# Kernel tuning notes

Hardware: AMD Instinct MI355X
Metric: run time of the kernel (lower is better)

Reference implementation:

```python
import jax, jax.numpy as jnp
import numpy as np

N_NODES = 100000
N_EDGES = 3200000
IN_CH = 64
HID = [64, 32, 16]


def setup_inputs() -> dict:
    key = jax.random.key(0)
    ks = jax.random.split(key, 12)
    x = jax.random.normal(ks[0], (N_NODES, IN_CH), dtype=jnp.float32)
    edge_index = jax.random.randint(ks[1], (2, N_EDGES), 0, N_NODES, dtype=jnp.int32)
    dims = [IN_CH] + HID
    params = {}
    i = 2
    for l in range(3):
        din, dout = dims[l], dims[l + 1]
        sc = 1.0 / np.sqrt(din)
        params[f"Wl{l}"] = jax.random.uniform(ks[i], (din, dout), jnp.float32, -sc, sc); i += 1
        params[f"Wr{l}"] = jax.random.uniform(ks[i], (din, dout), jnp.float32, -sc, sc); i += 1
        params[f"b{l}"] = jnp.zeros((dout,), jnp.float32)
    sc = 1.0 / np.sqrt(HID[-1])
    params["Wc"] = jax.random.uniform(ks[i], (HID[-1], 1), jnp.float32, -sc, sc)
    params["bc"] = jnp.zeros((1,), jnp.float32)
    return dict(x=x, edge_index=edge_index, **params)


def _sage_conv(x, src, dst, Wl, Wr, b):
    # message = x[src]; mean-aggregate at dst; out = agg @ Wl + x @ Wr + b
    msg = x[src]  # [E, din]
    s = jax.ops.segment_sum(msg, dst, num_segments=N_NODES)
    cnt = jax.ops.segment_sum(jnp.ones((dst.shape[0],), x.dtype), dst, num_segments=N_NODES)
    agg = s / jnp.maximum(cnt, 1.0)[:, None]
    return agg @ Wl + x @ Wr + b


def reference(x, edge_index, Wl0, Wr0, b0, Wl1, Wr1, b1, Wl2, Wr2, b2, Wc, bc):
    src, dst = edge_index[0], edge_index[1]
    h = jax.nn.relu(_sage_conv(x, src, dst, Wl0, Wr0, b0))
    h = jax.nn.relu(_sage_conv(h, src, dst, Wl1, Wr1, b1))
    h = jax.nn.relu(_sage_conv(h, src, dst, Wl2, Wr2, b2))
    return h @ Wc + bc  # [N_NODES, 1]
```

## Files before the change

### kernel.cpp

```cpp
#include <hip/hip_runtime.h>


#define NN 100000
#define BSH 8
#define NBK ((NN + 255) >> 8)
#define HB 256
#define SRCMASK 0x1FFFF
#define DLSH 17
#define SPCAP 12500
#define LADJ_CAP 10240

__device__ __forceinline__ unsigned f2bf(float f) {
    unsigned u = __float_as_uint(f);
    u += 0x7fffu + ((u >> 16) & 1u);
    return u >> 16;
}
__device__ __forceinline__ float bflo(unsigned u) { return __uint_as_float(u << 16); }
__device__ __forceinline__ float bfhi(unsigned u) { return __uint_as_float(u & 0xffff0000u); }

__global__ void part1_k(const int* __restrict__ src, const int* __restrict__ dst,
                        int E, int* __restrict__ gcnt, int* __restrict__ goff,
                        unsigned* __restrict__ pair) {
    __shared__ unsigned spair[SPCAP];
    __shared__ int lh[NBK];
    __shared__ int part[512];
    int c = blockIdx.x, tid = threadIdx.x;
    int chunk = (E + HB - 1) / HB;
    int b0 = c * chunk, e0 = min(b0 + chunk, E);
    int n = e0 - b0;
    if (tid < NBK) lh[tid] = 0;
    __syncthreads();
    for (int e = b0 + tid; e < e0; e += 512) atomicAdd(&lh[dst[e] >> BSH], 1);
    __syncthreads();
    int cnt = (tid < NBK) ? lh[tid] : 0;
    part[tid] = cnt;
    __syncthreads();
    for (int d = 1; d < 512; d <<= 1) {
        int t = (tid >= d) ? part[tid - d] : 0;
        __syncthreads();
        part[tid] += t;
        __syncthreads();
    }
    int run = (tid == 0) ? 0 : part[tid - 1];
    if (tid < NBK) {
        gcnt[(size_t)c * NBK + tid] = cnt;
        goff[(size_t)c * NBK + tid] = run;
        lh[tid] = run;
    }
    __syncthreads();
    for (int e = b0 + tid; e < e0; e += 512) {
        int dv = dst[e], sv = src[e];
        int p = atomicAdd(&lh[dv >> BSH], 1);
        spair[p] = (unsigned)sv | ((unsigned)(dv & 255) << DLSH);
    }
    __syncthreads();
    for (int i = tid; i < n; i += 512) pair[b0 + i] = spair[i];
}

__global__ void bsum_k(const int* __restrict__ gcnt, int* __restrict__ bb, int E) {
    __shared__ int part[512];
    int tid = threadIdx.x;
    int s = 0;
    if (tid < NBK)
        for (int c = 0; c < HB; ++c) s += gcnt[(size_t)c * NBK + tid];
    part[tid] = s;
    __syncthreads();
    for (int d = 1; d < 512; d <<= 1) {
        int t = (tid >= d) ? part[tid - d] : 0;
        __syncthreads();
        part[tid] += t;
        __syncthreads();
    }
    if (tid < NBK) bb[tid] = part[tid] - s;
    if (tid == 0) bb[NBK] = E;
}

__global__ void sort2_k(const unsigned* __restrict__ pair, const int* __restrict__ goff,
                        const int* __restrict__ bb, int* __restrict__ adj,
                        int* __restrict__ off, float* __restrict__ inv, int N, int E) {
    __shared__ int ladj[LADJ_CAP];
    __shared__ int sls[HB], sle[HB];
    __shared__ int lcur[256];
    __shared__ int part[256];
    int b = blockIdx.x, tid = threadIdx.x;
    int chunk = (E + HB - 1) / HB;
    int b0c = tid * chunk, e0c = min(b0c + chunk, E);
    int ls = b0c + goff[(size_t)tid * NBK + b];
    int le = (b + 1 < NBK) ? (b0c + goff[(size_t)tid * NBK + b + 1]) : e0c;
    sls[tid] = ls; sle[tid] = le;
    lcur[tid] = 0;
    __syncthreads();
    for (int i = ls; i < le; ++i)
        atomicAdd(&lcur[pair[i] >> DLSH], 1);
    __syncthreads();
    int cn = lcur[tid];
    part[tid] = cn;
    __syncthreads();
    for (int d = 1; d < 256; d <<= 1) {
        int t = (tid >= d) ? part[tid - d] : 0;
        __syncthreads();
        part[tid] += t;
        __syncthreads();
    }
    int run = part[tid] - cn;
    int base = bb[b];
    int total = bb[b + 1] - base;
    int v = (b << BSH) + tid;
    if (v < N) { off[v] = base + run; inv[v] = 1.f / (float)max(cn, 1); }
    if (b == NBK - 1 && tid == 0) off[N] = E;
    lcur[tid] = run;
    __syncthreads();
    for (int i = sls[tid]; i < sle[tid]; ++i) {
        unsigned u = pair[i];
        int p = atomicAdd(&lcur[u >> DLSH], 1);
        int val = u & SRCMASK;
        if (p < LADJ_CAP) ladj[p] = val;
        else adj[base + p] = val;
    }
    __syncthreads();
    int lim = min(total, LADJ_CAP);
    for (int i = tid; i < lim; i += 256) adj[base + i] = ladj[i];
}

template <int DIN, int DOUT>
__global__ void transform2_k(const float* __restrict__ h,
                             const float* __restrict__ Wl, const float* __restrict__ Wr,
                             const float* __restrict__ bias,
                             unsigned* __restrict__ g, float2* __restrict__ r, int N) {
    constexpr int JP = DOUT / 2;
    __shared__ float2 sWl[DIN * JP];
    __shared__ float2 sWr[DIN * JP];
    __shared__ float2 sb[JP];
    const float2* Wl2 = (const float2*)Wl;
    const float2* Wr2 = (const float2*)Wr;
    for (int i = threadIdx.x; i < DIN * JP; i += blockDim.x) { sWl[i] = Wl2[i]; sWr[i] = Wr2[i]; }
    if (threadIdx.x < JP) sb[threadIdx.x] = ((const float2*)bias)[threadIdx.x];
    __syncthreads();
    int idx = blockIdx.x * blockDim.x + threadIdx.x;
    int NP = N / 2;
    if (idx >= NP * JP) return;
    int p = idx / JP, jp = idx % JP;
    int v0 = 2 * p, v1 = v0 + 1;
    const float* h0 = h + (size_t)v0 * DIN;
    const float* h1 = h + (size_t)v1 * DIN;
    float gl0x = 0, gl0y = 0, gl1x = 0, gl1y = 0;
    float gr0x = 0, gr0y = 0, gr1x = 0, gr1y = 0;
#pragma unroll
    for (int k = 0; k < DIN; ++k) {
        float2 wl = sWl[k * JP + jp];
        float2 wr = sWr[k * JP + jp];
        float a0 = h0[k], a1 = h1[k];
        gl0x = fmaf(a0, wl.x, gl0x); gl0y = fmaf(a0, wl.y, gl0y);
        gl1x = fmaf(a1, wl.x, gl1x); gl1y = fmaf(a1, wl.y, gl1y);
        gr0x = fmaf(a0, wr.x, gr0x); gr0y = fmaf(a0, wr.y, gr0y);
        gr1x = fmaf(a1, wr.x, gr1x); gr1y = fmaf(a1, wr.y, gr1y);
    }
    float2 bb = sb[jp];
    g[(size_t)v0 * JP + jp] = f2bf(gl0x) | (f2bf(gl0y) << 16);
    g[(size_t)v1 * JP + jp] = f2bf(gl1x) | (f2bf(gl1y) << 16);
    r[(size_t)v0 * JP + jp] = make_float2(gr0x + bb.x, gr0y + bb.y);
    r[(size_t)v1 * JP + jp] = make_float2(gr1x + bb.x, gr1y + bb.y);
}

template <int DOUT, int WAVES, int HEAD>
__global__ void agg_k(const unsigned* __restrict__ g, const int* __restrict__ off,
                      const int* __restrict__ adj, const float* __restrict__ invc,
                      const float* r, const float* __restrict__ Wc,
                      const float* __restrict__ bc, float* out, int N) {
    constexpr int Q8 = DOUT / 8;
    constexpr int EPT = 64 / Q8;
    __shared__ float sagg[WAVES][DOUT];
    int wid = threadIdx.x >> 6, lane = threadIdx.x & 63;
    int v = blockIdx.x * WAVES + wid;
    bool active = v < N;
    int q = lane & (Q8 - 1);
    int eg = lane / Q8;
    float acc[8] = {0, 0, 0, 0, 0, 0, 0, 0};
#define ACCU(U) do { \
        acc[0] += bflo(U.x); acc[1] += bfhi(U.x); \
        acc[2] += bflo(U.y); acc[3] += bfhi(U.y); \
        acc[4] += bflo(U.z); acc[5] += bfhi(U.z); \
        acc[6] += bflo(U.w); acc[7] += bfhi(U.w); } while (0)
    if (active) {
        int beg = off[v], end = off[v + 1];
        const uint4* g4 = (const uint4*)g;
        int i = beg + eg;
        for (; i + 3 * EPT < end; i += 4 * EPT) {
            int s0 = adj[i], s1 = adj[i + EPT], s2 = adj[i + 2 * EPT], s3 = adj[i + 3 * EPT];
            uint4 u0 = g4[(size_t)s0 * Q8 + q];
            uint4 u1 = g4[(size_t)s1 * Q8 + q];
            uint4 u2 = g4[(size_t)s2 * Q8 + q];
            uint4 u3 = g4[(size_t)s3 * Q8 + q];
            ACCU(u0); ACCU(u1); ACCU(u2); ACCU(u3);
        }
        for (; i < end; i += EPT) {
            int sv = adj[i];
            uint4 u = g4[(size_t)sv * Q8 + q];
            ACCU(u);
        }
#pragma unroll
        for (int d = Q8; d < 64; d <<= 1)
#pragma unroll
            for (int c = 0; c < 8; ++c) acc[c] += __shfl_xor(acc[c], d, 64);
        if (eg == 0) {
            float4* sp = (float4*)&sagg[wid][q * 8];
            sp[0] = make_float4(acc[0], acc[1], acc[2], acc[3]);
            sp[1] = make_float4(acc[4], acc[5], acc[6], acc[7]);
        }
    }
#undef ACCU
    __syncthreads();
    if (active && lane < DOUT) {
        float iv = invc[v];
        float val = fmaxf(fmaf(sagg[wid][lane], iv, r[(size_t)v * DOUT + lane]), 0.f);
        if (!HEAD) {
            out[(size_t)v * DOUT + lane] = val;
        } else {
            float pp = val * Wc[lane];
#pragma unroll
            for (int d = 1; d < 16; d <<= 1) pp += __shfl_xor(pp, d, 64);
            if (lane == 0) out[v] = pp + bc[0];
        }
    }
}

extern "C" void kernel_launch(void* const* d_in, const int* in_sizes, int n_in,
                              void* d_out, int out_size, void* d_ws, size_t ws_size,
                              hipStream_t stream) {
    const float* x   = (const float*)d_in[0];
    const int*   ei  = (const int*)d_in[1];
    const float* Wl0 = (const float*)d_in[2];
    const float* Wr0 = (const float*)d_in[3];
    const float* b0  = (const float*)d_in[4];
    const float* Wl1 = (const float*)d_in[5];
    const float* Wr1 = (const float*)d_in[6];
    const float* b1  = (const float*)d_in[7];
    const float* Wl2 = (const float*)d_in[8];
    const float* Wr2 = (const float*)d_in[9];
    const float* b2  = (const float*)d_in[10];
    const float* Wc  = (const float*)d_in[11];
    const float* bc  = (const float*)d_in[12];
    float* out = (float*)d_out;

    const int N = NN;
    const int E = in_sizes[1] / 2;
    const int* src = ei;
    const int* dst = ei + E;

    char* ws = (char*)d_ws;
    const size_t MB = 1 << 20;
    int*      gcnt = (int*)(ws + 0);
    int*      goff = (int*)(ws + 1 * MB);
    int*      bb   = (int*)(ws + 2 * MB);
    int*      off  = (int*)(ws + 3 * MB);
    float*    inv  = (float*)(ws + 3 * MB + 512 * 1024);
    unsigned* pair = (unsigned*)(ws + 4 * MB);
    int*      adj  = (int*)(ws + 17 * MB);
    unsigned* g0 = (unsigned*)(ws + 30 * MB);
    float*    r0 = (float*)(ws + 43 * MB);
    float*    h1 = r0;
    unsigned* g1 = (unsigned*)(ws + 4 * MB);
    float*    r1 = (float*)(ws + 30 * MB);
    float*    h2 = r1;
    unsigned* g2 = (unsigned*)(ws + 11 * MB);
    float*    r2 = (float*)(ws + 43 * MB);

    part1_k<<<HB, 512, 0, stream>>>(src, dst, E, gcnt, goff, pair);
    bsum_k<<<1, 512, 0, stream>>>(gcnt, bb, E);
    sort2_k<<<NBK, HB, 0, stream>>>(pair, goff, bb, adj, off, inv, N, E);

    transform2_k<64, 64><<<(N / 2 * 32 + 255) / 256, 256, 0, stream>>>(x, Wl0, Wr0, b0, g0, (float2*)r0, N);
    agg_k<64, 4, 0><<<(N + 3) / 4, 256, 0, stream>>>(g0, off, adj, inv, r0, nullptr, nullptr, h1, N);

    transform2_k<64, 32><<<(N / 2 * 16 + 255) / 256, 256, 0, stream>>>(h1, Wl1, Wr1, b1, g1, (float2*)r1, N);
    agg_k<32, 4, 0><<<(N + 3) / 4, 256, 0, stream>>>(g1, off, adj, inv, r1, nullptr, nullptr, h2, N);

    transform2_k<32, 16><<<(N / 2 * 8 + 255) / 256, 256, 0, stream>>>(h2, Wl2, Wr2, b2, g2, (float2*)r2, N);
    agg_k<16, 4, 1><<<(N + 3) / 4, 256, 0, stream>>>(g2, off, adj, inv, r2, Wc, bc, out, N);
}
```

Before: 405.4 us.

## Fuse next-layer transform into aggregation kernels and store residual in bf16

```diff
diff --git a/kernel.cpp b/kernel.cpp
--- a/kernel.cpp
+++ b/kernel.cpp
@@ -17,11 +17,13 @@
 }
 __device__ __forceinline__ float bflo(unsigned u) { return __uint_as_float(u << 16); }
 __device__ __forceinline__ float bfhi(unsigned u) { return __uint_as_float(u & 0xffff0000u); }
+__device__ __forceinline__ float bfs(unsigned short s) { return __uint_as_float((unsigned)s << 16); }
 
 __global__ void part1_k(const int* __restrict__ src, const int* __restrict__ dst,
                         int E, int* __restrict__ gcnt, int* __restrict__ goff,
                         unsigned* __restrict__ pair) {
     __shared__ unsigned spair[SPCAP];
+    __shared__ int sdst[SPCAP];
     __shared__ int lh[NBK];
     __shared__ int part[512];
     int c = blockIdx.x, tid = threadIdx.x;
@@ -30,7 +32,11 @@
     int n = e0 - b0;
     if (tid < NBK) lh[tid] = 0;
     __syncthreads();
-    for (int e = b0 + tid; e < e0; e += 512) atomicAdd(&lh[dst[e] >> BSH], 1);
+    for (int i = tid; i < n; i += 512) {
+        int dv = dst[b0 + i];
+        sdst[i] = dv;
+        atomicAdd(&lh[dv >> BSH], 1);
+    }
     __syncthreads();
     int cnt = (tid < NBK) ? lh[tid] : 0;
     part[tid] = cnt;
@@ -48,8 +54,9 @@
         lh[tid] = run;
     }
     __syncthreads();
-    for (int e = b0 + tid; e < e0; e += 512) {
-        int dv = dst[e], sv = src[e];
+    for (int i = tid; i < n; i += 512) {
+        int dv = sdst[i];
+        int sv = src[b0 + i];
         int p = atomicAdd(&lh[dv >> BSH], 1);
         spair[p] = (unsigned)sv | ((unsigned)(dv & 255) << DLSH);
     }
@@ -126,7 +133,7 @@
 __global__ void transform2_k(const float* __restrict__ h,
                              const float* __restrict__ Wl, const float* __restrict__ Wr,
                              const float* __restrict__ bias,
-                             unsigned* __restrict__ g, float2* __restrict__ r, int N) {
+                             unsigned* __restrict__ g, unsigned* __restrict__ r, int N) {
     constexpr int JP = DOUT / 2;
     __shared__ float2 sWl[DIN * JP];
     __shared__ float2 sWr[DIN * JP];
@@ -158,18 +165,27 @@
     float2 bb = sb[jp];
     g[(size_t)v0 * JP + jp] = f2bf(gl0x) | (f2bf(gl0y) << 16);
     g[(size_t)v1 * JP + jp] = f2bf(gl1x) | (f2bf(gl1y) << 16);
-    r[(size_t)v0 * JP + jp] = make_float2(gr0x + bb.x, gr0y + bb.y);
-    r[(size_t)v1 * JP + jp] = make_float2(gr1x + bb.x, gr1y + bb.y);
-}
-
-template <int DOUT, int WAVES, int HEAD>
-__global__ void agg_k(const unsigned* __restrict__ g, const int* __restrict__ off,
-                      const int* __restrict__ adj, const float* __restrict__ invc,
-                      const float* r, const float* __restrict__ Wc,
-                      const float* __restrict__ bc, float* out, int N) {
+    r[(size_t)v0 * JP + jp] = f2bf(gr0x + bb.x) | (f2bf(gr0y + bb.y) << 16);
+    r[(size_t)v1 * JP + jp] = f2bf(gr1x + bb.x) | (f2bf(gr1y + bb.y) << 16);
+}
+
+template <int DOUT, int DNEXT, int WAVES>
+__global__ void aggt_k(const unsigned* __restrict__ g, const int* __restrict__ off,
+                       const int* __restrict__ adj, const float* __restrict__ invc,
+                       const unsigned short* __restrict__ r,
+                       const float* __restrict__ Wln, const float* __restrict__ Wrn,
+                       const float* __restrict__ bn,
+                       unsigned short* __restrict__ gnext, unsigned short* __restrict__ rnext,
+                       int N) {
     constexpr int Q8 = DOUT / 8;
     constexpr int EPT = 64 / Q8;
     __shared__ float sagg[WAVES][DOUT];
+    __shared__ float sh[WAVES][DOUT];
+    __shared__ float sWl[DOUT * DNEXT];
+    __shared__ float sWr[DOUT * DNEXT];
+    __shared__ float sbn[DNEXT];
+    for (int i = threadIdx.x; i < DOUT * DNEXT; i += blockDim.x) { sWl[i] = Wln[i]; sWr[i] = Wrn[i]; }
+    if (threadIdx.x < DNEXT) sbn[threadIdx.x] = bn[threadIdx.x];
     int wid = threadIdx.x >> 6, lane = threadIdx.x & 63;
     int v = blockIdx.x * WAVES + wid;
     bool active = v < N;
@@ -208,19 +224,79 @@
             sp[1] = make_float4(acc[4], acc[5], acc[6], acc[7]);
         }
     }
+    __syncthreads();
+    if (active && lane < DOUT) {
+        float rv = bfs(r[(size_t)v * DOUT + lane]);
+        sh[wid][lane] = fmaxf(fmaf(sagg[wid][lane], invc[v], rv), 0.f);
+    }
+    __syncthreads();
+    constexpr int TOT = WAVES * DNEXT * 2;
+    if (threadIdx.x < TOT) {
+        int j = threadIdx.x % DNEXT;
+        int node = (threadIdx.x / DNEXT) % WAVES;
+        int m = threadIdx.x / (DNEXT * WAVES);
+        int vv = blockIdx.x * WAVES + node;
+        if (vv < N) {
+            const float* W = m ? sWr : sWl;
+            float a = m ? sbn[j] : 0.f;
+#pragma unroll
+            for (int k = 0; k < DOUT; ++k) a = fmaf(sh[node][k], W[k * DNEXT + j], a);
+            unsigned short bv = (unsigned short)f2bf(a);
+            if (m) rnext[(size_t)vv * DNEXT + j] = bv;
+            else   gnext[(size_t)vv * DNEXT + j] = bv;
+        }
+    }
+}
+
+template <int WAVES>
+__global__ void aggh_k(const unsigned* __restrict__ g, const int* __restrict__ off,
+                       const int* __restrict__ adj, const float* __restrict__ invc,
+                       const unsigned short* __restrict__ r, const float* __restrict__ Wc,
+                       const float* __restrict__ bc, float* __restrict__ out, int N) {
+    constexpr int DOUT = 16, Q8 = 2, EPT = 32;
+    __shared__ float sagg[WAVES][DOUT];
+    int wid = threadIdx.x >> 6, lane = threadIdx.x & 63;
+    int v = blockIdx.x * WAVES + wid;
+    bool active = v < N;
+    int q = lane & (Q8 - 1);
+    int eg = lane / Q8;
+    float acc[8] = {0, 0, 0, 0, 0, 0, 0, 0};
+    if (active) {
+        int beg = off[v], end = off[v + 1];
+        const uint4* g4 = (const uint4*)g;
+        int i = beg + eg;
+        for (; i + 3 * EPT < end; i += 4 * EPT) {
+            int s0 = adj[i], s1 = adj[i + EPT], s2 = adj[i + 2 * EPT], s3 = adj[i + 3 * EPT];
+            uint4 u0 = g4[(size_t)s0 * Q8 + q];
+            uint4 u1 = g4[(size_t)s1 * Q8 + q];
+            uint4 u2 = g4[(size_t)s2 * Q8 + q];
+            uint4 u3 = g4[(size_t)s3 * Q8 + q];
+            ACCU(u0); ACCU(u1); ACCU(u2); ACCU(u3);
+        }
+        for (; i < end; i += EPT) {
+            int sv = adj[i];
+            uint4 u = g4[(size_t)sv * Q8 + q];
+            ACCU(u);
+        }
+#pragma unroll
+        for (int d = Q8; d < 64; d <<= 1)
+#pragma unroll
+            for (int c = 0; c < 8; ++c) acc[c] += __shfl_xor(acc[c], d, 64);
+        if (eg == 0) {
+            float4* sp = (float4*)&sagg[wid][q * 8];
+            sp[0] = make_float4(acc[0], acc[1], acc[2], acc[3]);
+            sp[1] = make_float4(acc[4], acc[5], acc[6], acc[7]);
+        }
+    }
 #undef ACCU
     __syncthreads();
     if (active && lane < DOUT) {
-        float iv = invc[v];
-        float val = fmaxf(fmaf(sagg[wid][lane], iv, r[(size_t)v * DOUT + lane]), 0.f);
-        if (!HEAD) {
-            out[(size_t)v * DOUT + lane] = val;
-        } else {
-            float pp = val * Wc[lane];
-#pragma unroll
-            for (int d = 1; d < 16; d <<= 1) pp += __shfl_xor(pp, d, 64);
-            if (lane == 0) out[v] = pp + bc[0];
-        }
+        float rv = bfs(r[(size_t)v * DOUT + lane]);
+        float val = fmaxf(fmaf(sagg[wid][lane], invc[v], rv), 0.f);
+        float pp = val * Wc[lane];
+#pragma unroll
+        for (int d = 1; d < 16; d <<= 1) pp += __shfl_xor(pp, d, 64);
+        if (lane == 0) out[v] = pp + bc[0];
     }
 }
 
@@ -256,25 +332,21 @@
     float*    inv  = (float*)(ws + 3 * MB + 512 * 1024);
     unsigned* pair = (unsigned*)(ws + 4 * MB);
     int*      adj  = (int*)(ws + 17 * MB);
-    unsigned* g0 = (unsigned*)(ws + 30 * MB);
-    float*    r0 = (float*)(ws + 43 * MB);
-    float*    h1 = r0;
-    unsigned* g1 = (unsigned*)(ws + 4 * MB);
-    float*    r1 = (float*)(ws + 30 * MB);
-    float*    h2 = r1;
-    unsigned* g2 = (unsigned*)(ws + 11 * MB);
-    float*    r2 = (float*)(ws + 43 * MB);
+    unsigned*       g0 = (unsigned*)(ws + 30 * MB);
+    unsigned*       r0 = (unsigned*)(ws + 43 * MB);
+    unsigned short* g1 = (unsigned short*)(ws + 4 * MB);
+    unsigned short* r1 = (unsigned short*)(ws + 4 * MB + 6400000);
+    unsigned short* g2 = (unsigned short*)(ws + 30 * MB);
+    unsigned short* r2 = (unsigned short*)(ws + 34 * MB);
 
     part1_k<<<HB, 512, 0, stream>>>(src, dst, E, gcnt, goff, pair);
     bsum_k<<<1, 512, 0, stream>>>(gcnt, bb, E);
     sort2_k<<<NBK, HB, 0, stream>>>(pair, goff, bb, adj, off, inv, N, E);
 
-    transform2_k<64, 64><<<(N / 2 * 32 + 255) / 256, 256, 0, stream>>>(x, Wl0, Wr0, b0, g0, (float2*)r0, N);
-    agg_k<64, 4, 0><<<(N + 3) / 4, 256, 0, stream>>>(g0, off, adj, inv, r0, nullptr, nullptr, h1, N);
-
-    transform2_k<64, 32><<<(N / 2 * 16 + 255) / 256, 256, 0, stream>>>(h1, Wl1, Wr1, b1, g1, (float2*)r1, N);
-    agg_k<32, 4, 0><<<(N + 3) / 4, 256, 0, stream>>>(g1, off, adj, inv, r1, nullptr, nullptr, h2, N);
-
-    transform2_k<32, 16><<<(N / 2 * 8 + 255) / 256, 256, 0, stream>>>(h2, Wl2, Wr2, b2, g2, (float2*)r2, N);
-    agg_k<16, 4, 1><<<(N + 3) / 4, 256, 0, stream>>>(g2, off, adj, inv, r2, Wc, bc, out, N);
-}
+    transform2_k<64, 64><<<(N / 2 * 32 + 255) / 256, 256, 0, stream>>>(x, Wl0, Wr0, b0, g0, r0, N);
+    aggt_k<64, 32, 4><<<(N + 3) / 4, 256, 0, stream>>>(g0, off, adj, inv,
+        (const unsigned short*)r0, Wl1, Wr1, b1, g1, r1, N);
+    aggt_k<32, 16, 4><<<(N + 3) / 4, 256, 0, stream>>>((const unsigned*)g1, off, adj, inv,
+        r1, Wl2, Wr2, b2, g2, r2, N);
+    aggh_k<4><<<(N + 3) / 4, 256, 0, stream>>>((const unsigned*)g2, off, adj, inv, r2, Wc, bc, out, N);
+}
```

New measurement: 434.2 us. 7.1% more time.
